# Kernel tuning notes

Hardware: AMD Instinct MI355X
Metric: run time of the kernel (lower is better)

Reference implementation:

```python
import jax, jax.numpy as jnp
import numpy as np

C = 512
NUM_HEADS = 8
HEAD_DIM = C // NUM_HEADS


def setup_inputs() -> dict:
    key = jax.random.key(0)
    ks = jax.random.split(key, 9)
    s = 1.0 / np.sqrt(C)
    x = jax.random.normal(ks[0], (8, C, 32, 32), dtype=jnp.float32)
    Wq = jax.random.uniform(ks[1], (C, C), jnp.float32, -s, s)
    bq = jax.random.uniform(ks[2], (C,), jnp.float32, -s, s)
    Wk = jax.random.uniform(ks[3], (C, C), jnp.float32, -s, s)
    bk = jax.random.uniform(ks[4], (C,), jnp.float32, -s, s)
    Wv = jax.random.uniform(ks[5], (C, C), jnp.float32, -s, s)
    bv = jax.random.uniform(ks[6], (C,), jnp.float32, -s, s)
    Wo = jax.random.uniform(ks[7], (C, C), jnp.float32, -s, s)
    bo = jax.random.uniform(ks[8], (C,), jnp.float32, -s, s)
    return {"x": x, "Wq": Wq, "bq": bq, "Wk": Wk, "bk": bk,
            "Wv": Wv, "bv": bv, "Wo": Wo, "bo": bo}


def reference(x, Wq, bq, Wk, bk, Wv, bv, Wo, bo):
    N, Cc, H, W = x.shape
    S = H * W
    # [N, S, C] token sequence
    xs = x.reshape(N, Cc, S).transpose(0, 2, 1)
    # torch Linear: y = x @ W^T + b
    q = xs @ Wq.T + bq
    k = xs @ Wk.T + bk
    v = xs @ Wv.T + bv
    # [N, h, S, d]
    q = q.reshape(N, S, NUM_HEADS, HEAD_DIM).transpose(0, 2, 1, 3)
    k = k.reshape(N, S, NUM_HEADS, HEAD_DIM).transpose(0, 2, 1, 3)
    v = v.reshape(N, S, NUM_HEADS, HEAD_DIM).transpose(0, 2, 1, 3)
    energy = jnp.einsum('nhqd,nhkd->nhqk', q, k)
    attn = jax.nn.softmax(energy / np.sqrt(HEAD_DIM), axis=3)
    out = jnp.einsum('nhql,nhld->nhqd', attn, v)
    # back to [N, S, C]; note torch reshape from (N,h,S,d) order
    out = out.reshape(N, Cc, S) if False else out.reshape(N, -1, Cc)
    out = out @ Wo.T + bo
    return out.reshape(N, Cc, H, W)


if __name__ == "__main__":
    o = reference(**setup_inputs())
    print(o.shape)
```

## Files before the change

kernel.cpp:

```cpp
#include <hip/hip_runtime.h>


typedef _Float16 f16x8 __attribute__((ext_vector_type(8)));
typedef _Float16 f16x4 __attribute__((ext_vector_type(4)));
typedef float f32x4 __attribute__((ext_vector_type(4)));

__device__ inline void gl_lds16(const void* g, void* l) {
  __builtin_amdgcn_global_load_lds((const __attribute__((address_space(1))) void*)g,
                                   (__attribute__((address_space(3))) void*)l, 16, 0, 0);
}

__device__ inline float fexp2(float x) {
#if __has_builtin(__builtin_amdgcn_exp2f)
  return __builtin_amdgcn_exp2f(x);
#else
  return exp2f(x);
#endif
}

__global__ void prep(const float* __restrict__ x,
                     const float* __restrict__ Wq, const float* __restrict__ bq,
                     const float* __restrict__ Wk, const float* __restrict__ bk,
                     const float* __restrict__ Wv, const float* __restrict__ bv,
                     const float* __restrict__ Wo,
                     _Float16* __restrict__ xs16, _Float16* __restrict__ Wqkv16,
                     float* __restrict__ bqkv, _Float16* __restrict__ Wo16) {
  __shared__ float t[32][33];
  const int tid = threadIdx.x;
  if (blockIdx.x < 1024) {
    const float g = 0.18033688011112042f;
    int i = blockIdx.x * 256 + tid;
    Wqkv16[i]          = (_Float16)(Wq[i] * g);
    Wqkv16[262144 + i] = (_Float16)Wk[i];
    Wqkv16[524288 + i] = (_Float16)Wv[i];
    Wo16[i]            = (_Float16)Wo[i];
    if (i < 512) {
      bqkv[i]        = bq[i] * g;
      bqkv[512 + i]  = bk[i];
      bqkv[1024 + i] = bv[i];
    }
    return;
  }
  const int bid = blockIdx.x - 1024;
  const int n = bid >> 9, c0 = ((bid >> 5) & 15) * 32, s0 = (bid & 31) * 32;
  const int tx = tid & 31, ty = tid >> 5;
#pragma unroll
  for (int i = 0; i < 4; ++i) {
    int cc = ty + i * 8;
    t[cc][tx] = x[((size_t)n * 512 + c0 + cc) * 1024 + s0 + tx];
  }
  __syncthreads();
#pragma unroll
  for (int i = 0; i < 4; ++i) {
    int ss = ty + i * 8;
    xs16[((size_t)n * 1024 + s0 + ss) * 512 + c0 + tx] = (_Float16)t[tx][ss];
  }
}

__global__ __launch_bounds__(256, 2) void qkv_gemm(
    const _Float16* __restrict__ A, const _Float16* __restrict__ Bw,
    const float* __restrict__ bias, _Float16* __restrict__ QK,
    _Float16* __restrict__ Vt) {
  __shared__ _Float16 smem[16896];
  _Float16* As = smem;
  _Float16* Bs = smem + 4096;
  const int tid = threadIdx.x;
  const int lane = tid & 63, w = tid >> 6;
  const int quad = lane >> 4, l15 = lane & 15;
  const int bm = blockIdx.x * 128, bn = blockIdx.y * 128;
  const int wr = (w >> 1) * 64, wc = (w & 1) * 64;
  f32x4 acc[4][4] = {};
  for (int k0 = 0; k0 < 512; k0 += 32) {
    __syncthreads();
#pragma unroll
    for (int c = 0; c < 2; ++c) {
      int idx = c * 256 + tid;
      int row = idx >> 2, sc = idx & 3;
      int kg = sc ^ ((row >> 1) & 3);
      gl_lds16(A + (size_t)(bm + row) * 512 + k0 + kg * 8, As + idx * 8);
      gl_lds16(Bw + (size_t)(bn + row) * 512 + k0 + kg * 8, Bs + idx * 8);
    }
    __syncthreads();
    f16x8 af[4], bf[4];
#pragma unroll
    for (int i = 0; i < 4; ++i) {
      int ra = wr + i * 16 + l15;
      af[i] = *(const f16x8*)(As + ra * 32 + (quad ^ ((ra >> 1) & 3)) * 8);
      int rb = wc + i * 16 + l15;
      bf[i] = *(const f16x8*)(Bs + rb * 32 + (quad ^ ((rb >> 1) & 3)) * 8);
    }
#pragma unroll
    for (int i = 0; i < 4; ++i)
#pragma unroll
      for (int j = 0; j < 4; ++j)
        acc[i][j] = __builtin_amdgcn_mfma_f32_16x16x32_f16(af[i], bf[j], acc[i][j], 0, 0, 0);
  }
  if (blockIdx.y < 8) {
#pragma unroll
    for (int j = 0; j < 4; ++j) {
      int col = bn + wc + j * 16 + l15;
      float bb = bias[col];
#pragma unroll
      for (int i = 0; i < 4; ++i) {
        int rowb = bm + wr + i * 16 + quad * 4;
#pragma unroll
        for (int r = 0; r < 4; ++r)
          QK[(size_t)(rowb + r) * 1024 + col] = (_Float16)(acc[i][j][r] + bb);
      }
    }
  } else {
    __syncthreads();
#pragma unroll
    for (int j = 0; j < 4; ++j) {
      int cl = wc + j * 16 + l15;
      float bb = bias[bn + cl];
#pragma unroll
      for (int i = 0; i < 4; ++i) {
        int row = wr + i * 16 + quad * 4;
        f16x4 pk;
#pragma unroll
        for (int r = 0; r < 4; ++r) pk[r] = (_Float16)(acc[i][j][r] + bb);
        *(f16x4*)(smem + cl * 132 + row) = pk;
      }
    }
    __syncthreads();
    const int n = bm >> 10, s0g = bm & 1023;
    const int vh = (bn - 1024) >> 6;
    const int cl = tid >> 1, par = tid & 1;
    const int hh = vh + (cl >> 6), d = cl & 63;
    const size_t vrow = (((size_t)((n * 8 + hh) * 64 + d)) << 10) + s0g;
#pragma unroll
    for (int g = 0; g < 8; ++g) {
      int pb = g * 16 + par * 8;
      int a32 = pb & ~31, q = (pb >> 3) & 3;
      f16x4 lo = *(const f16x4*)(smem + cl * 132 + a32 + 4 * q);
      f16x4 hi = *(const f16x4*)(smem + cl * 132 + a32 + 16 + 4 * q);
      f16x8 o = {lo[0], lo[1], lo[2], lo[3], hi[0], hi[1], hi[2], hi[3]};
      *(f16x8*)(Vt + vrow + pb) = o;
    }
  }
}

__global__ __launch_bounds__(256, 2) void attn(
    const _Float16* __restrict__ QK, const _Float16* __restrict__ Vt,
    _Float16* __restrict__ O16) {
  __shared__ _Float16 Qs[128 * 64];
  __shared__ _Float16 Ks[128 * 64];
  __shared__ _Float16 Vs[64 * 128];
  const int tid = threadIdx.x, lane = tid & 63, w = tid >> 6;
  const int quad = lane >> 4, l15 = lane & 15;
  const int n = blockIdx.y >> 3, h = blockIdx.y & 7;
  const int q0 = blockIdx.x * 128;
#pragma unroll
  for (int c = 0; c < 4; ++c) {
    int idx = c * 256 + tid;
    int row = idx >> 3, sc = idx & 7;
    int dg = sc ^ (row & 7);
    gl_lds16(QK + (size_t)(n * 1024 + q0 + row) * 1024 + h * 64 + dg * 8, Qs + idx * 8);
  }
  __syncthreads();
  f16x8 qf[2][2];
#pragma unroll
  for (int mt = 0; mt < 2; ++mt)
#pragma unroll
    for (int dc = 0; dc < 2; ++dc) {
      int row = w * 32 + mt * 16 + l15;
      qf[mt][dc] = *(const f16x8*)(Qs + row * 64 + ((dc * 4 + quad) ^ (row & 7)) * 8);
    }
  f32x4 oacc[2][4] = {};
  f32x4 lsum[2] = {};
  const f16x8 ones = {(_Float16)1, (_Float16)1, (_Float16)1, (_Float16)1,
                      (_Float16)1, (_Float16)1, (_Float16)1, (_Float16)1};

  for (int kt = 0; kt < 8; ++kt) {
    __syncthreads();
#pragma unroll
    for (int c = 0; c < 4; ++c) {
      int idx = c * 256 + tid;
      int row = idx >> 3, sck = idx & 7;
      int dg = sck ^ (row & 7);
      gl_lds16(QK + (size_t)(n * 1024 + kt * 128 + row) * 1024 + 512 + h * 64 + dg * 8,
               Ks + idx * 8);
      int d = idx >> 4, scv = idx & 15;
      int vg = scv ^ (d & 7);
      gl_lds16(Vt + (size_t)((n * 8 + h) * 64 + d) * 1024 + kt * 128 + vg * 8,
               Vs + idx * 8);
    }
    __syncthreads();
#pragma unroll
    for (int sc = 0; sc < 4; ++sc) {
      f32x4 sacc[2][2] = {};
#pragma unroll
      for (int t = 0; t < 2; ++t) {
        int rk = (sc * 2 + t) * 16 + l15;
        f16x8 kf0 = *(const f16x8*)(Ks + rk * 64 + ((quad) ^ (rk & 7)) * 8);
        f16x8 kf1 = *(const f16x8*)(Ks + rk * 64 + ((4 + quad) ^ (rk & 7)) * 8);
#pragma unroll
        for (int mt = 0; mt < 2; ++mt) {
          sacc[mt][t] = __builtin_amdgcn_mfma_f32_16x16x32_f16(kf0, qf[mt][0], sacc[mt][t], 0, 0, 0);
          sacc[mt][t] = __builtin_amdgcn_mfma_f32_16x16x32_f16(kf1, qf[mt][1], sacc[mt][t], 0, 0, 0);
        }
      }
      f16x8 pf[2];
#pragma unroll
      for (int mt = 0; mt < 2; ++mt) {
#pragma unroll
        for (int t = 0; t < 2; ++t)
#pragma unroll
          for (int r = 0; r < 4; ++r)
            pf[mt][t * 4 + r] = (_Float16)fexp2(sacc[mt][t][r]);
        lsum[mt] = __builtin_amdgcn_mfma_f32_16x16x32_f16(pf[mt], ones, lsum[mt], 0, 0, 0);
      }
#pragma unroll
      for (int nt = 0; nt < 4; ++nt) {
        int rd = nt * 16 + l15;
        f16x8 vf = *(const f16x8*)(Vs + rd * 128 + ((sc * 4 + quad) ^ (rd & 7)) * 8);
#pragma unroll
        for (int mt = 0; mt < 2; ++mt)
          oacc[mt][nt] = __builtin_amdgcn_mfma_f32_16x16x32_f16(pf[mt], vf, oacc[mt][nt], 0, 0, 0);
      }
    }
  }
#pragma unroll
  for (int mt = 0; mt < 2; ++mt) {
#pragma unroll
    for (int r = 0; r < 4; ++r) {
      float rinv = 1.0f / lsum[mt][r];
      int s = q0 + w * 32 + mt * 16 + quad * 4 + r;
      int i = h * 128 + (s >> 3);
      int jb = (s & 7) * 64;
#pragma unroll
      for (int nt = 0; nt < 4; ++nt) {
        int d = nt * 16 + l15;
        O16[(size_t)(n * 1024 + i) * 512 + jb + d] = (_Float16)(oacc[mt][nt][r] * rinv);
      }
    }
  }
}

__global__ __launch_bounds__(256, 2) void out_gemm(
    const _Float16* __restrict__ A, const _Float16* __restrict__ Bw,
    const float* __restrict__ bias, float* __restrict__ out) {
  __shared__ _Float16 As[128 * 32];
  __shared__ _Float16 Bs[128 * 32];
  const int tid = threadIdx.x;
  const int lane = tid & 63, w = tid >> 6;
  const int quad = lane >> 4, l15 = lane & 15;
  const int bm = blockIdx.x * 128, bn = blockIdx.y * 128;
  const int wr = (w >> 1) * 64, wc = (w & 1) * 64;
  f32x4 acc[4][4] = {};
  for (int k0 = 0; k0 < 512; k0 += 32) {
    __syncthreads();
#pragma unroll
    for (int c = 0; c < 2; ++c) {
      int idx = c * 256 + tid;
      int row = idx >> 2, sc = idx & 3;
      int kg = sc ^ ((row >> 1) & 3);
      gl_lds16(A + (size_t)(bm + row) * 512 + k0 + kg * 8, As + idx * 8);
      gl_lds16(Bw + (size_t)(bn + row) * 512 + k0 + kg * 8, Bs + idx * 8);
    }
    __syncthreads();
    f16x8 af[4], bf[4];
#pragma unroll
    for (int i = 0; i < 4; ++i) {
      int ra = wr + i * 16 + l15;
      af[i] = *(const f16x8*)(As + ra * 32 + (quad ^ ((ra >> 1) & 3)) * 8);
      int rb = wc + i * 16 + l15;
      bf[i] = *(const f16x8*)(Bs + rb * 32 + (quad ^ ((rb >> 1) & 3)) * 8);
    }
#pragma unroll
    for (int i = 0; i < 4; ++i)
#pragma unroll
      for (int j = 0; j < 4; ++j)
        acc[i][j] = __builtin_amdgcn_mfma_f32_16x16x32_f16(af[i], bf[j], acc[i][j], 0, 0, 0);
  }
#pragma unroll
  for (int j = 0; j < 4; ++j) {
    int col = bn + wc + j * 16 + l15;
    float bb = bias[col];
#pragma unroll
    for (int i = 0; i < 4; ++i) {
      int rowb = bm + wr + i * 16 + quad * 4;
#pragma unroll
      for (int r = 0; r < 4; ++r)
        out[(size_t)(rowb + r) * 512 + col] = acc[i][j][r] + bb;
    }
  }
}

extern "C" void kernel_launch(void* const* d_in, const int* in_sizes, int n_in,
                              void* d_out, int out_size, void* d_ws, size_t ws_size,
                              hipStream_t stream) {
  const float* x  = (const float*)d_in[0];
  const float* Wq = (const float*)d_in[1];
  const float* bq = (const float*)d_in[2];
  const float* Wk = (const float*)d_in[3];
  const float* bk = (const float*)d_in[4];
  const float* Wv = (const float*)d_in[5];
  const float* bv = (const float*)d_in[6];
  const float* Wo = (const float*)d_in[7];
  const float* bo = (const float*)d_in[8];
  float* out = (float*)d_out;
  char* ws = (char*)d_ws;

  _Float16* xs16   = (_Float16*)(ws);
  _Float16* QK     = (_Float16*)(ws + (8u << 20));
  _Float16* Vt     = (_Float16*)(ws + (24u << 20));
  _Float16* Wqkv16 = (_Float16*)(ws + (32u << 20));
  _Float16* Wo16   = (_Float16*)(ws + (32u << 20) + 1572864);
  float*    bqkv   = (float*)   (ws + (32u << 20) + 2097152);

  hipLaunchKernelGGL(prep, dim3(5120), dim3(256), 0, stream,
                     x, Wq, bq, Wk, bk, Wv, bv, Wo, xs16, Wqkv16, bqkv, Wo16);
  hipLaunchKernelGGL(qkv_gemm, dim3(64, 12), dim3(256), 0, stream,
                     xs16, Wqkv16, bqkv, QK, Vt);
  hipLaunchKernelGGL(attn, dim3(8, 64), dim3(256), 0, stream, QK, Vt, xs16);
  hipLaunchKernelGGL(out_gemm, dim3(64, 4), dim3(256), 0, stream,
                     xs16, Wo16, bo, out);
}
```

Baseline: 144.6 us.

## Fuse fp32-to-fp16 conversion and transpose into GEMMs, dropping prep kernel

Removes the separate prep kernel. The QKV GEMM now reads fp32 x and weights directly, transposes and converts them in registers, and writes them to double-buffered LDS, prefetching the next K slice. The output GEMM likewise converts Wo on the fly and double-buffers A. The attention epilogue swaps the MFMA operand order so each lane writes vectorized f16x4 outputs, using a shuffle to fetch row sums. This saves a launch and a round trip of the converted data through memory, at the cost of more register pressure and repeated weight conversion in every block.

Measured after the change: 163.5 us. 1.13x slower.

```diff
diff --git a/kernel.cpp b/kernel.cpp
--- a/kernel.cpp
+++ b/kernel.cpp
@@ -3,6 +3,7 @@
 
 typedef _Float16 f16x8 __attribute__((ext_vector_type(8)));
 typedef _Float16 f16x4 __attribute__((ext_vector_type(4)));
+typedef _Float16 f16x2 __attribute__((ext_vector_type(2)));
 typedef float f32x4 __attribute__((ext_vector_type(4)));
 
 __device__ inline void gl_lds16(const void* g, void* l) {
@@ -18,69 +19,80 @@
 #endif
 }
 
-__global__ void prep(const float* __restrict__ x,
-                     const float* __restrict__ Wq, const float* __restrict__ bq,
-                     const float* __restrict__ Wk, const float* __restrict__ bk,
-                     const float* __restrict__ Wv, const float* __restrict__ bv,
-                     const float* __restrict__ Wo,
-                     _Float16* __restrict__ xs16, _Float16* __restrict__ Wqkv16,
-                     float* __restrict__ bqkv, _Float16* __restrict__ Wo16) {
-  __shared__ float t[32][33];
-  const int tid = threadIdx.x;
-  if (blockIdx.x < 1024) {
-    const float g = 0.18033688011112042f;
-    int i = blockIdx.x * 256 + tid;
-    Wqkv16[i]          = (_Float16)(Wq[i] * g);
-    Wqkv16[262144 + i] = (_Float16)Wk[i];
-    Wqkv16[524288 + i] = (_Float16)Wv[i];
-    Wo16[i]            = (_Float16)Wo[i];
-    if (i < 512) {
-      bqkv[i]        = bq[i] * g;
-      bqkv[512 + i]  = bk[i];
-      bqkv[1024 + i] = bv[i];
-    }
-    return;
-  }
-  const int bid = blockIdx.x - 1024;
-  const int n = bid >> 9, c0 = ((bid >> 5) & 15) * 32, s0 = (bid & 31) * 32;
-  const int tx = tid & 31, ty = tid >> 5;
-#pragma unroll
-  for (int i = 0; i < 4; ++i) {
-    int cc = ty + i * 8;
-    t[cc][tx] = x[((size_t)n * 512 + c0 + cc) * 1024 + s0 + tx];
-  }
-  __syncthreads();
-#pragma unroll
-  for (int i = 0; i < 4; ++i) {
-    int ss = ty + i * 8;
-    xs16[((size_t)n * 1024 + s0 + ss) * 512 + c0 + tx] = (_Float16)t[tx][ss];
-  }
-}
-
 __global__ __launch_bounds__(256, 2) void qkv_gemm(
-    const _Float16* __restrict__ A, const _Float16* __restrict__ Bw,
-    const float* __restrict__ bias, _Float16* __restrict__ QK,
-    _Float16* __restrict__ Vt) {
+    const float* __restrict__ x,
+    const float* __restrict__ Wq, const float* __restrict__ Wk,
+    const float* __restrict__ Wv,
+    const float* __restrict__ bq, const float* __restrict__ bk,
+    const float* __restrict__ bv,
+    _Float16* __restrict__ QK, _Float16* __restrict__ Vt) {
   __shared__ _Float16 smem[16896];
-  _Float16* As = smem;
-  _Float16* Bs = smem + 4096;
   const int tid = threadIdx.x;
   const int lane = tid & 63, w = tid >> 6;
   const int quad = lane >> 4, l15 = lane & 15;
-  const int bm = blockIdx.x * 128, bn = blockIdx.y * 128;
+  const int bn = blockIdx.x * 128, bm = blockIdx.y * 128;
   const int wr = (w >> 1) * 64, wc = (w & 1) * 64;
+  const int n = bm >> 10, s_base = bm & 1023;
+  const float g = 0.18033688011112042f;
+  const float* Wsel = (bn < 512) ? Wq : (bn < 1024 ? Wk : Wv);
+  const float* bsel = (bn < 512) ? bq : (bn < 1024 ? bk : bv);
+  const int row0 = bn & 511;
+  const float gw = (bn < 512) ? g : 1.0f;
+
+  const int cpr = (tid >> 4) * 2;
+  const int s8 = (tid & 15) * 8;
+  const int wrow = tid >> 1;
+  const int wh = (tid & 1) * 16;
+
+  float av[16], wv16[16];
   f32x4 acc[4][4] = {};
-  for (int k0 = 0; k0 < 512; k0 += 32) {
-    __syncthreads();
+
+  {
+    const float* xs = x + ((size_t)(n * 512 + cpr) * 1024) + s_base + s8;
+    *(float4*)(av + 0) = *(const float4*)(xs);
+    *(float4*)(av + 4) = *(const float4*)(xs + 4);
+    *(float4*)(av + 8) = *(const float4*)(xs + 1024);
+    *(float4*)(av + 12) = *(const float4*)(xs + 1028);
+    const float* ws = Wsel + (size_t)(row0 + wrow) * 512 + wh;
+    *(float4*)(wv16 + 0) = *(const float4*)(ws);
+    *(float4*)(wv16 + 4) = *(const float4*)(ws + 4);
+    *(float4*)(wv16 + 8) = *(const float4*)(ws + 8);
+    *(float4*)(wv16 + 12) = *(const float4*)(ws + 12);
+  }
+  for (int ki = 0; ki < 16; ++ki) {
+    const int buf = ki & 1;
+    _Float16* As = smem + buf * 8192;
+    _Float16* Bs = smem + buf * 8192 + 4096;
+#pragma unroll
+    for (int i = 0; i < 8; ++i) {
+      int s_l = s8 + i;
+      int slot = (cpr >> 3) ^ ((s_l >> 1) & 3);
+      f16x2 pk = {(_Float16)av[i], (_Float16)av[8 + i]};
+      *(f16x2*)(As + s_l * 32 + slot * 8 + (cpr & 7)) = pk;
+    }
 #pragma unroll
     for (int c = 0; c < 2; ++c) {
-      int idx = c * 256 + tid;
-      int row = idx >> 2, sc = idx & 3;
-      int kg = sc ^ ((row >> 1) & 3);
-      gl_lds16(A + (size_t)(bm + row) * 512 + k0 + kg * 8, As + idx * 8);
-      gl_lds16(Bw + (size_t)(bn + row) * 512 + k0 + kg * 8, Bs + idx * 8);
-    }
-    __syncthreads();
+      int jc = (tid & 1) * 2 + c;
+      int slot = jc ^ ((wrow >> 1) & 3);
+      f16x8 pk;
+#pragma unroll
+      for (int j = 0; j < 8; ++j) pk[j] = (_Float16)(wv16[c * 8 + j] * gw);
+      *(f16x8*)(Bs + wrow * 32 + slot * 8) = pk;
+    }
+    __syncthreads();
+    if (ki < 15) {
+      int k0 = (ki + 1) * 32;
+      const float* xs = x + ((size_t)(n * 512 + k0 + cpr) * 1024) + s_base + s8;
+      *(float4*)(av + 0) = *(const float4*)(xs);
+      *(float4*)(av + 4) = *(const float4*)(xs + 4);
+      *(float4*)(av + 8) = *(const float4*)(xs + 1024);
+      *(float4*)(av + 12) = *(const float4*)(xs + 1028);
+      const float* ws = Wsel + (size_t)(row0 + wrow) * 512 + k0 + wh;
+      *(float4*)(wv16 + 0) = *(const float4*)(ws);
+      *(float4*)(wv16 + 4) = *(const float4*)(ws + 4);
+      *(float4*)(wv16 + 8) = *(const float4*)(ws + 8);
+      *(float4*)(wv16 + 12) = *(const float4*)(ws + 12);
+    }
     f16x8 af[4], bf[4];
 #pragma unroll
     for (int i = 0; i < 4; ++i) {
@@ -94,12 +106,14 @@
 #pragma unroll
       for (int j = 0; j < 4; ++j)
         acc[i][j] = __builtin_amdgcn_mfma_f32_16x16x32_f16(af[i], bf[j], acc[i][j], 0, 0, 0);
-  }
-  if (blockIdx.y < 8) {
+    __syncthreads();
+  }
+  if (bn < 1024) {
 #pragma unroll
     for (int j = 0; j < 4; ++j) {
-      int col = bn + wc + j * 16 + l15;
-      float bb = bias[col];
+      int cl = wc + j * 16 + l15;
+      float bb = bsel[(bn & 511) + cl] * gw;
+      int col = bn + cl;
 #pragma unroll
       for (int i = 0; i < 4; ++i) {
         int rowb = bm + wr + i * 16 + quad * 4;
@@ -113,7 +127,7 @@
 #pragma unroll
     for (int j = 0; j < 4; ++j) {
       int cl = wc + j * 16 + l15;
-      float bb = bias[bn + cl];
+      float bb = bsel[cl + (bn & 511)];
 #pragma unroll
       for (int i = 0; i < 4; ++i) {
         int row = wr + i * 16 + quad * 4;
@@ -124,14 +138,14 @@
       }
     }
     __syncthreads();
-    const int n = bm >> 10, s0g = bm & 1023;
+    const int s0g = bm & 1023;
     const int vh = (bn - 1024) >> 6;
     const int cl = tid >> 1, par = tid & 1;
     const int hh = vh + (cl >> 6), d = cl & 63;
     const size_t vrow = (((size_t)((n * 8 + hh) * 64 + d)) << 10) + s0g;
 #pragma unroll
-    for (int g = 0; g < 8; ++g) {
-      int pb = g * 16 + par * 8;
+    for (int gq = 0; gq < 8; ++gq) {
+      int pb = gq * 16 + par * 8;
       int a32 = pb & ~31, q = (pb >> 3) & 3;
       f16x4 lo = *(const f16x4*)(smem + cl * 132 + a32 + 4 * q);
       f16x4 hi = *(const f16x4*)(smem + cl * 132 + a32 + 16 + 4 * q);
@@ -167,7 +181,7 @@
       int row = w * 32 + mt * 16 + l15;
       qf[mt][dc] = *(const f16x8*)(Qs + row * 64 + ((dc * 4 + quad) ^ (row & 7)) * 8);
     }
-  f32x4 oacc[2][4] = {};
+  f32x4 oaccT[4][2] = {};
   f32x4 lsum[2] = {};
   const f16x8 ones = {(_Float16)1, (_Float16)1, (_Float16)1, (_Float16)1,
                       (_Float16)1, (_Float16)1, (_Float16)1, (_Float16)1};
@@ -217,49 +231,88 @@
         f16x8 vf = *(const f16x8*)(Vs + rd * 128 + ((sc * 4 + quad) ^ (rd & 7)) * 8);
 #pragma unroll
         for (int mt = 0; mt < 2; ++mt)
-          oacc[mt][nt] = __builtin_amdgcn_mfma_f32_16x16x32_f16(pf[mt], vf, oacc[mt][nt], 0, 0, 0);
+          oaccT[nt][mt] = __builtin_amdgcn_mfma_f32_16x16x32_f16(vf, pf[mt], oaccT[nt][mt], 0, 0, 0);
       }
     }
   }
 #pragma unroll
   for (int mt = 0; mt < 2; ++mt) {
-#pragma unroll
-    for (int r = 0; r < 4; ++r) {
-      float rinv = 1.0f / lsum[mt][r];
-      int s = q0 + w * 32 + mt * 16 + quad * 4 + r;
-      int i = h * 128 + (s >> 3);
-      int jb = (s & 7) * 64;
-#pragma unroll
-      for (int nt = 0; nt < 4; ++nt) {
-        int d = nt * 16 + l15;
-        O16[(size_t)(n * 1024 + i) * 512 + jb + d] = (_Float16)(oacc[mt][nt][r] * rinv);
-      }
+    int r3 = l15 & 3;
+    float lv = lsum[mt][0];
+    lv = (r3 == 1) ? lsum[mt][1] : lv;
+    lv = (r3 == 2) ? lsum[mt][2] : lv;
+    lv = (r3 == 3) ? lsum[mt][3] : lv;
+    float lq = __shfl(lv, (l15 >> 2) * 16 + (l15 & 3), 64);
+    float rinv = 1.0f / lq;
+    int q = q0 + w * 32 + mt * 16 + l15;
+    int i = h * 128 + (q >> 3);
+    size_t base = (size_t)(n * 1024 + i) * 512 + (q & 7) * 64 + quad * 4;
+#pragma unroll
+    for (int nt = 0; nt < 4; ++nt) {
+      f16x4 pk;
+#pragma unroll
+      for (int r = 0; r < 4; ++r) pk[r] = (_Float16)(oaccT[nt][mt][r] * rinv);
+      *(f16x4*)(O16 + base + nt * 16) = pk;
     }
   }
 }
 
 __global__ __launch_bounds__(256, 2) void out_gemm(
-    const _Float16* __restrict__ A, const _Float16* __restrict__ Bw,
-    const float* __restrict__ bias, float* __restrict__ out) {
-  __shared__ _Float16 As[128 * 32];
-  __shared__ _Float16 Bs[128 * 32];
+    const _Float16* __restrict__ A, const float* __restrict__ Wo,
+    const float* __restrict__ bo, float* __restrict__ out) {
+  __shared__ _Float16 smem[16384];
   const int tid = threadIdx.x;
   const int lane = tid & 63, w = tid >> 6;
   const int quad = lane >> 4, l15 = lane & 15;
   const int bm = blockIdx.x * 128, bn = blockIdx.y * 128;
   const int wr = (w >> 1) * 64, wc = (w & 1) * 64;
+  const int wrow = tid >> 1, wh = (tid & 1) * 16;
+  float wv16[16];
   f32x4 acc[4][4] = {};
-  for (int k0 = 0; k0 < 512; k0 += 32) {
-    __syncthreads();
+  {
 #pragma unroll
     for (int c = 0; c < 2; ++c) {
       int idx = c * 256 + tid;
       int row = idx >> 2, sc = idx & 3;
       int kg = sc ^ ((row >> 1) & 3);
-      gl_lds16(A + (size_t)(bm + row) * 512 + k0 + kg * 8, As + idx * 8);
-      gl_lds16(Bw + (size_t)(bn + row) * 512 + k0 + kg * 8, Bs + idx * 8);
-    }
-    __syncthreads();
+      gl_lds16(A + (size_t)(bm + row) * 512 + kg * 8, smem + idx * 8);
+    }
+    const float* ws = Wo + (size_t)(bn + wrow) * 512 + wh;
+    *(float4*)(wv16 + 0) = *(const float4*)(ws);
+    *(float4*)(wv16 + 4) = *(const float4*)(ws + 4);
+    *(float4*)(wv16 + 8) = *(const float4*)(ws + 8);
+    *(float4*)(wv16 + 12) = *(const float4*)(ws + 12);
+  }
+  for (int ki = 0; ki < 16; ++ki) {
+    const int buf = ki & 1;
+    _Float16* As = smem + buf * 8192;
+    _Float16* Bs = smem + buf * 8192 + 4096;
+#pragma unroll
+    for (int c = 0; c < 2; ++c) {
+      int jc = (tid & 1) * 2 + c;
+      int slot = jc ^ ((wrow >> 1) & 3);
+      f16x8 pk;
+#pragma unroll
+      for (int j = 0; j < 8; ++j) pk[j] = (_Float16)wv16[c * 8 + j];
+      *(f16x8*)(Bs + wrow * 32 + slot * 8) = pk;
+    }
+    __syncthreads();
+    if (ki < 15) {
+      int k0 = (ki + 1) * 32;
+      _Float16* Asn = smem + (1 - buf) * 8192;
+#pragma unroll
+      for (int c = 0; c < 2; ++c) {
+        int idx = c * 256 + tid;
+        int row = idx >> 2, sc = idx & 3;
+        int kg = sc ^ ((row >> 1) & 3);
+        gl_lds16(A + (size_t)(bm + row) * 512 + k0 + kg * 8, Asn + idx * 8);
+      }
+      const float* ws = Wo + (size_t)(bn + wrow) * 512 + k0 + wh;
+      *(float4*)(wv16 + 0) = *(const float4*)(ws);
+      *(float4*)(wv16 + 4) = *(const float4*)(ws + 4);
+      *(float4*)(wv16 + 8) = *(const float4*)(ws + 8);
+      *(float4*)(wv16 + 12) = *(const float4*)(ws + 12);
+    }
     f16x8 af[4], bf[4];
 #pragma unroll
     for (int i = 0; i < 4; ++i) {
@@ -273,11 +326,12 @@
 #pragma unroll
       for (int j = 0; j < 4; ++j)
         acc[i][j] = __builtin_amdgcn_mfma_f32_16x16x32_f16(af[i], bf[j], acc[i][j], 0, 0, 0);
+    __syncthreads();
   }
 #pragma unroll
   for (int j = 0; j < 4; ++j) {
     int col = bn + wc + j * 16 + l15;
-    float bb = bias[col];
+    float bb = bo[col];
 #pragma unroll
     for (int i = 0; i < 4; ++i) {
       int rowb = bm + wr + i * 16 + quad * 4;
@@ -303,18 +357,13 @@
   float* out = (float*)d_out;
   char* ws = (char*)d_ws;
 
-  _Float16* xs16   = (_Float16*)(ws);
-  _Float16* QK     = (_Float16*)(ws + (8u << 20));
-  _Float16* Vt     = (_Float16*)(ws + (24u << 20));
-  _Float16* Wqkv16 = (_Float16*)(ws + (32u << 20));
-  _Float16* Wo16   = (_Float16*)(ws + (32u << 20) + 1572864);
-  float*    bqkv   = (float*)   (ws + (32u << 20) + 2097152);
-
-  hipLaunchKernelGGL(prep, dim3(5120), dim3(256), 0, stream,
-                     x, Wq, bq, Wk, bk, Wv, bv, Wo, xs16, Wqkv16, bqkv, Wo16);
-  hipLaunchKernelGGL(qkv_gemm, dim3(64, 12), dim3(256), 0, stream,
-                     xs16, Wqkv16, bqkv, QK, Vt);
-  hipLaunchKernelGGL(attn, dim3(8, 64), dim3(256), 0, stream, QK, Vt, xs16);
+  _Float16* QK  = (_Float16*)(ws);
+  _Float16* Vt  = (_Float16*)(ws + (16u << 20));
+  _Float16* O16 = (_Float16*)(ws + (24u << 20));
+
+  hipLaunchKernelGGL(qkv_gemm, dim3(12, 64), dim3(256), 0, stream,
+                     x, Wq, Wk, Wv, bq, bk, bv, QK, Vt);
+  hipLaunchKernelGGL(attn, dim3(8, 64), dim3(256), 0, stream, QK, Vt, O16);
   hipLaunchKernelGGL(out_gemm, dim3(64, 4), dim3(256), 0, stream,
-                     xs16, Wo16, bo, out);
-}
+                     O16, Wo, bo, out);
+}
```

## Store Q/K/V in MFMA-fragment-packed layout and drop LDS staging in attention

Applied to the files above, without the earlier changes.

The QKV GEMM epilogue now writes Q, K and V into per-head buffers pre-swizzled in the exact order the MFMA fragments are consumed. The attention kernel can then load each fragment straight from global memory with one contiguous 16-byte load per lane, with no LDS staging and no barriers. The PV product is also transposed so the output can be written as packed f16x4 stores, with the row sums moved across lanes by a shuffle. In exchange K and V are reread from global or L2 by every wave without LDS sharing, and the epilogue does scattered LDS gathers. The attention output also gets its own buffer instead of overwriting xs16.

Result: slower. 168.0 us (+16.2%).

```diff
diff --git a/kernel.cpp b/kernel.cpp
--- a/kernel.cpp
+++ b/kernel.cpp
@@ -59,8 +59,8 @@
 
 __global__ __launch_bounds__(256, 2) void qkv_gemm(
     const _Float16* __restrict__ A, const _Float16* __restrict__ Bw,
-    const float* __restrict__ bias, _Float16* __restrict__ QK,
-    _Float16* __restrict__ Vt) {
+    const float* __restrict__ bias, _Float16* __restrict__ Qp,
+    _Float16* __restrict__ Kp, _Float16* __restrict__ Vp) {
   __shared__ _Float16 smem[16896];
   _Float16* As = smem;
   _Float16* Bs = smem + 4096;
@@ -95,106 +95,92 @@
       for (int j = 0; j < 4; ++j)
         acc[i][j] = __builtin_amdgcn_mfma_f32_16x16x32_f16(af[i], bf[j], acc[i][j], 0, 0, 0);
   }
-  if (blockIdx.y < 8) {
-#pragma unroll
-    for (int j = 0; j < 4; ++j) {
-      int col = bn + wc + j * 16 + l15;
-      float bb = bias[col];
-#pragma unroll
-      for (int i = 0; i < 4; ++i) {
-        int rowb = bm + wr + i * 16 + quad * 4;
-#pragma unroll
-        for (int r = 0; r < 4; ++r)
-          QK[(size_t)(rowb + r) * 1024 + col] = (_Float16)(acc[i][j][r] + bb);
+  __syncthreads();
+#pragma unroll
+  for (int j = 0; j < 4; ++j) {
+    int cl = wc + j * 16 + l15;
+    float bb = bias[bn + cl];
+#pragma unroll
+    for (int i = 0; i < 4; ++i) {
+      int row = wr + i * 16 + quad * 4;
+      f16x4 pk;
+#pragma unroll
+      for (int r = 0; r < 4; ++r) pk[r] = (_Float16)(acc[i][j][r] + bb);
+      *(f16x4*)(smem + cl * 132 + row) = pk;
+    }
+  }
+  __syncthreads();
+  const int cls = bn >> 9;
+  const int h0 = (bn & 511) >> 6;
+  const int n = bm >> 10, s_base = bm & 1023;
+  _Float16* dst = (cls == 0) ? Qp : (cls == 1) ? Kp : Vp;
+  if (cls < 2) {
+#pragma unroll
+    for (int c = 0; c < 8; ++c) {
+      int id = c * 256 + tid;
+      int l15p = id & 15, qd = (id >> 4) & 3, th = (id >> 6) & 1;
+      int s16l = (id >> 7) & 7, h2 = id >> 10;
+      int f_loc = h2 * 64 + th * 32 + qd * 8;
+      int s_loc = s16l * 16 + l15p;
+      f16x8 v;
+#pragma unroll
+      for (int j = 0; j < 8; ++j) v[j] = smem[(f_loc + j) * 132 + s_loc];
+      size_t off = (size_t)(n * 8 + h0 + h2) * 65536 +
+                   (size_t)((s_base >> 4) + s16l) * 1024 + th * 512 + qd * 128 + l15p * 8;
+      *(f16x8*)(dst + off) = v;
+    }
+  } else {
+    const int kt = s_base >> 7;
+#pragma unroll
+    for (int c = 0; c < 8; ++c) {
+      int id = c * 256 + tid;
+      int l15d = id & 15, qd = (id >> 4) & 3, nt = (id >> 6) & 3;
+      int sc = (id >> 8) & 3, h2 = id >> 10;
+      int f_loc = h2 * 64 + nt * 16 + l15d;
+      f16x8 v;
+#pragma unroll
+      for (int j = 0; j < 8; ++j) {
+        int s_loc = sc * 32 + (j >> 2) * 16 + qd * 4 + (j & 3);
+        v[j] = smem[f_loc * 132 + s_loc];
       }
-    }
-  } else {
-    __syncthreads();
-#pragma unroll
-    for (int j = 0; j < 4; ++j) {
-      int cl = wc + j * 16 + l15;
-      float bb = bias[bn + cl];
-#pragma unroll
-      for (int i = 0; i < 4; ++i) {
-        int row = wr + i * 16 + quad * 4;
-        f16x4 pk;
-#pragma unroll
-        for (int r = 0; r < 4; ++r) pk[r] = (_Float16)(acc[i][j][r] + bb);
-        *(f16x4*)(smem + cl * 132 + row) = pk;
-      }
-    }
-    __syncthreads();
-    const int n = bm >> 10, s0g = bm & 1023;
-    const int vh = (bn - 1024) >> 6;
-    const int cl = tid >> 1, par = tid & 1;
-    const int hh = vh + (cl >> 6), d = cl & 63;
-    const size_t vrow = (((size_t)((n * 8 + hh) * 64 + d)) << 10) + s0g;
-#pragma unroll
-    for (int g = 0; g < 8; ++g) {
-      int pb = g * 16 + par * 8;
-      int a32 = pb & ~31, q = (pb >> 3) & 3;
-      f16x4 lo = *(const f16x4*)(smem + cl * 132 + a32 + 4 * q);
-      f16x4 hi = *(const f16x4*)(smem + cl * 132 + a32 + 16 + 4 * q);
-      f16x8 o = {lo[0], lo[1], lo[2], lo[3], hi[0], hi[1], hi[2], hi[3]};
-      *(f16x8*)(Vt + vrow + pb) = o;
+      size_t off = (size_t)(n * 8 + h0 + h2) * 65536 + kt * 8192 +
+                   sc * 2048 + nt * 512 + qd * 128 + l15d * 8;
+      *(f16x8*)(dst + off) = v;
     }
   }
 }
 
 __global__ __launch_bounds__(256, 2) void attn(
-    const _Float16* __restrict__ QK, const _Float16* __restrict__ Vt,
-    _Float16* __restrict__ O16) {
-  __shared__ _Float16 Qs[128 * 64];
-  __shared__ _Float16 Ks[128 * 64];
-  __shared__ _Float16 Vs[64 * 128];
+    const _Float16* __restrict__ Qp, const _Float16* __restrict__ Kp,
+    const _Float16* __restrict__ Vp, _Float16* __restrict__ O16) {
   const int tid = threadIdx.x, lane = tid & 63, w = tid >> 6;
   const int quad = lane >> 4, l15 = lane & 15;
-  const int n = blockIdx.y >> 3, h = blockIdx.y & 7;
+  const int nh = blockIdx.y;
+  const int n = nh >> 3, h = nh & 7;
   const int q0 = blockIdx.x * 128;
-#pragma unroll
-  for (int c = 0; c < 4; ++c) {
-    int idx = c * 256 + tid;
-    int row = idx >> 3, sc = idx & 7;
-    int dg = sc ^ (row & 7);
-    gl_lds16(QK + (size_t)(n * 1024 + q0 + row) * 1024 + h * 64 + dg * 8, Qs + idx * 8);
-  }
-  __syncthreads();
+  const _Float16* Qb = Qp + (size_t)nh * 65536;
+  const _Float16* Kb = Kp + (size_t)nh * 65536;
+  const _Float16* Vb = Vp + (size_t)nh * 65536;
+  const int LL = lane * 8;
   f16x8 qf[2][2];
 #pragma unroll
   for (int mt = 0; mt < 2; ++mt)
 #pragma unroll
-    for (int dc = 0; dc < 2; ++dc) {
-      int row = w * 32 + mt * 16 + l15;
-      qf[mt][dc] = *(const f16x8*)(Qs + row * 64 + ((dc * 4 + quad) ^ (row & 7)) * 8);
-    }
-  f32x4 oacc[2][4] = {};
+    for (int th = 0; th < 2; ++th)
+      qf[mt][th] = *(const f16x8*)(Qb + (q0 / 16 + w * 2 + mt) * 1024 + th * 512 + LL);
+  f32x4 oaccT[4][2] = {};
   f32x4 lsum[2] = {};
   const f16x8 ones = {(_Float16)1, (_Float16)1, (_Float16)1, (_Float16)1,
                       (_Float16)1, (_Float16)1, (_Float16)1, (_Float16)1};
-
   for (int kt = 0; kt < 8; ++kt) {
-    __syncthreads();
-#pragma unroll
-    for (int c = 0; c < 4; ++c) {
-      int idx = c * 256 + tid;
-      int row = idx >> 3, sck = idx & 7;
-      int dg = sck ^ (row & 7);
-      gl_lds16(QK + (size_t)(n * 1024 + kt * 128 + row) * 1024 + 512 + h * 64 + dg * 8,
-               Ks + idx * 8);
-      int d = idx >> 4, scv = idx & 15;
-      int vg = scv ^ (d & 7);
-      gl_lds16(Vt + (size_t)((n * 8 + h) * 64 + d) * 1024 + kt * 128 + vg * 8,
-               Vs + idx * 8);
-    }
-    __syncthreads();
 #pragma unroll
     for (int sc = 0; sc < 4; ++sc) {
       f32x4 sacc[2][2] = {};
 #pragma unroll
       for (int t = 0; t < 2; ++t) {
-        int rk = (sc * 2 + t) * 16 + l15;
-        f16x8 kf0 = *(const f16x8*)(Ks + rk * 64 + ((quad) ^ (rk & 7)) * 8);
-        f16x8 kf1 = *(const f16x8*)(Ks + rk * 64 + ((4 + quad) ^ (rk & 7)) * 8);
+        int s16 = kt * 8 + sc * 2 + t;
+        f16x8 kf0 = *(const f16x8*)(Kb + s16 * 1024 + LL);
+        f16x8 kf1 = *(const f16x8*)(Kb + s16 * 1024 + 512 + LL);
 #pragma unroll
         for (int mt = 0; mt < 2; ++mt) {
           sacc[mt][t] = __builtin_amdgcn_mfma_f32_16x16x32_f16(kf0, qf[mt][0], sacc[mt][t], 0, 0, 0);
@@ -213,27 +199,31 @@
       }
 #pragma unroll
       for (int nt = 0; nt < 4; ++nt) {
-        int rd = nt * 16 + l15;
-        f16x8 vf = *(const f16x8*)(Vs + rd * 128 + ((sc * 4 + quad) ^ (rd & 7)) * 8);
+        f16x8 vf = *(const f16x8*)(Vb + kt * 8192 + sc * 2048 + nt * 512 + LL);
 #pragma unroll
         for (int mt = 0; mt < 2; ++mt)
-          oacc[mt][nt] = __builtin_amdgcn_mfma_f32_16x16x32_f16(pf[mt], vf, oacc[mt][nt], 0, 0, 0);
+          oaccT[nt][mt] = __builtin_amdgcn_mfma_f32_16x16x32_f16(vf, pf[mt], oaccT[nt][mt], 0, 0, 0);
       }
     }
   }
 #pragma unroll
   for (int mt = 0; mt < 2; ++mt) {
-#pragma unroll
-    for (int r = 0; r < 4; ++r) {
-      float rinv = 1.0f / lsum[mt][r];
-      int s = q0 + w * 32 + mt * 16 + quad * 4 + r;
-      int i = h * 128 + (s >> 3);
-      int jb = (s & 7) * 64;
-#pragma unroll
-      for (int nt = 0; nt < 4; ++nt) {
-        int d = nt * 16 + l15;
-        O16[(size_t)(n * 1024 + i) * 512 + jb + d] = (_Float16)(oacc[mt][nt][r] * rinv);
-      }
+    int r3 = l15 & 3;
+    float lv = lsum[mt][0];
+    lv = (r3 == 1) ? lsum[mt][1] : lv;
+    lv = (r3 == 2) ? lsum[mt][2] : lv;
+    lv = (r3 == 3) ? lsum[mt][3] : lv;
+    float lq = __shfl(lv, (l15 >> 2) * 16 + (l15 & 3), 64);
+    float rinv = 1.0f / lq;
+    int q = q0 + w * 32 + mt * 16 + l15;
+    int i = h * 128 + (q >> 3);
+    size_t base = (size_t)(n * 1024 + i) * 512 + (q & 7) * 64 + quad * 4;
+#pragma unroll
+    for (int nt = 0; nt < 4; ++nt) {
+      f16x4 pk;
+#pragma unroll
+      for (int r = 0; r < 4; ++r) pk[r] = (_Float16)(oaccT[nt][mt][r] * rinv);
+      *(f16x4*)(O16 + base + nt * 16) = pk;
     }
   }
 }
@@ -304,17 +294,19 @@
   char* ws = (char*)d_ws;
 
   _Float16* xs16   = (_Float16*)(ws);
-  _Float16* QK     = (_Float16*)(ws + (8u << 20));
-  _Float16* Vt     = (_Float16*)(ws + (24u << 20));
-  _Float16* Wqkv16 = (_Float16*)(ws + (32u << 20));
-  _Float16* Wo16   = (_Float16*)(ws + (32u << 20) + 1572864);
-  float*    bqkv   = (float*)   (ws + (32u << 20) + 2097152);
+  _Float16* O16    = (_Float16*)(ws + (8u << 20));
+  _Float16* Qp     = (_Float16*)(ws + (16u << 20));
+  _Float16* Kp     = (_Float16*)(ws + (24u << 20));
+  _Float16* Vp     = (_Float16*)(ws + (32u << 20));
+  _Float16* Wqkv16 = (_Float16*)(ws + (40u << 20));
+  _Float16* Wo16   = (_Float16*)(ws + (40u << 20) + 1572864);
+  float*    bqkv   = (float*)   (ws + (40u << 20) + 2097152);
 
   hipLaunchKernelGGL(prep, dim3(5120), dim3(256), 0, stream,
                      x, Wq, bq, Wk, bk, Wv, bv, Wo, xs16, Wqkv16, bqkv, Wo16);
   hipLaunchKernelGGL(qkv_gemm, dim3(64, 12), dim3(256), 0, stream,
-                     xs16, Wqkv16, bqkv, QK, Vt);
-  hipLaunchKernelGGL(attn, dim3(8, 64), dim3(256), 0, stream, QK, Vt, xs16);
+                     xs16, Wqkv16, bqkv, Qp, Kp, Vp);
+  hipLaunchKernelGGL(attn, dim3(8, 64), dim3(256), 0, stream, Qp, Kp, Vp, O16);
   hipLaunchKernelGGL(out_gemm, dim3(64, 4), dim3(256), 0, stream,
-                     xs16, Wo16, bo, out);
-}
+                     O16, Wo16, bo, out);
+}
```

## Deepen QKV GEMM k-tile to 64 and vectorize attention output stores

Applied to the files above, without the earlier changes.

The QKV projection GEMM now stages 64-wide K slices instead of 32, with a matching 8-way XOR swizzle. This halves the number of barrier and load rounds per tile and issues two MFMA sub-steps per stage. The attention kernel computes the transposed P·V product (V as the A operand), so each lane holds four consecutive head-dim values. It can then write packed f16x4 stores instead of scattered scalar halves, and the row sums are fetched with a lane shuffle. The larger LDS footprint per block could reduce occupancy.

After: 142.3 us. No clear change (-1.6%).

```diff
diff --git a/kernel.cpp b/kernel.cpp
--- a/kernel.cpp
+++ b/kernel.cpp
@@ -63,37 +63,40 @@
     _Float16* __restrict__ Vt) {
   __shared__ _Float16 smem[16896];
   _Float16* As = smem;
-  _Float16* Bs = smem + 4096;
+  _Float16* Bs = smem + 8192;
   const int tid = threadIdx.x;
   const int lane = tid & 63, w = tid >> 6;
   const int quad = lane >> 4, l15 = lane & 15;
   const int bm = blockIdx.x * 128, bn = blockIdx.y * 128;
   const int wr = (w >> 1) * 64, wc = (w & 1) * 64;
   f32x4 acc[4][4] = {};
-  for (int k0 = 0; k0 < 512; k0 += 32) {
-    __syncthreads();
-#pragma unroll
-    for (int c = 0; c < 2; ++c) {
+  for (int k0 = 0; k0 < 512; k0 += 64) {
+    __syncthreads();
+#pragma unroll
+    for (int c = 0; c < 4; ++c) {
       int idx = c * 256 + tid;
-      int row = idx >> 2, sc = idx & 3;
-      int kg = sc ^ ((row >> 1) & 3);
+      int row = idx >> 3, sc = idx & 7;
+      int kg = sc ^ (row & 7);
       gl_lds16(A + (size_t)(bm + row) * 512 + k0 + kg * 8, As + idx * 8);
       gl_lds16(Bw + (size_t)(bn + row) * 512 + k0 + kg * 8, Bs + idx * 8);
     }
     __syncthreads();
-    f16x8 af[4], bf[4];
-#pragma unroll
-    for (int i = 0; i < 4; ++i) {
-      int ra = wr + i * 16 + l15;
-      af[i] = *(const f16x8*)(As + ra * 32 + (quad ^ ((ra >> 1) & 3)) * 8);
-      int rb = wc + i * 16 + l15;
-      bf[i] = *(const f16x8*)(Bs + rb * 32 + (quad ^ ((rb >> 1) & 3)) * 8);
-    }
-#pragma unroll
-    for (int i = 0; i < 4; ++i)
-#pragma unroll
-      for (int j = 0; j < 4; ++j)
-        acc[i][j] = __builtin_amdgcn_mfma_f32_16x16x32_f16(af[i], bf[j], acc[i][j], 0, 0, 0);
+#pragma unroll
+    for (int kh = 0; kh < 2; ++kh) {
+      f16x8 af[4], bf[4];
+#pragma unroll
+      for (int i = 0; i < 4; ++i) {
+        int ra = wr + i * 16 + l15;
+        af[i] = *(const f16x8*)(As + ra * 64 + ((kh * 4 + quad) ^ (ra & 7)) * 8);
+        int rb = wc + i * 16 + l15;
+        bf[i] = *(const f16x8*)(Bs + rb * 64 + ((kh * 4 + quad) ^ (rb & 7)) * 8);
+      }
+#pragma unroll
+      for (int i = 0; i < 4; ++i)
+#pragma unroll
+        for (int j = 0; j < 4; ++j)
+          acc[i][j] = __builtin_amdgcn_mfma_f32_16x16x32_f16(af[i], bf[j], acc[i][j], 0, 0, 0);
+    }
   }
   if (blockIdx.y < 8) {
 #pragma unroll
@@ -167,7 +170,7 @@
       int row = w * 32 + mt * 16 + l15;
       qf[mt][dc] = *(const f16x8*)(Qs + row * 64 + ((dc * 4 + quad) ^ (row & 7)) * 8);
     }
-  f32x4 oacc[2][4] = {};
+  f32x4 oaccT[4][2] = {};
   f32x4 lsum[2] = {};
   const f16x8 ones = {(_Float16)1, (_Float16)1, (_Float16)1, (_Float16)1,
                       (_Float16)1, (_Float16)1, (_Float16)1, (_Float16)1};
@@ -217,23 +220,28 @@
         f16x8 vf = *(const f16x8*)(Vs + rd * 128 + ((sc * 4 + quad) ^ (rd & 7)) * 8);
 #pragma unroll
         for (int mt = 0; mt < 2; ++mt)
-          oacc[mt][nt] = __builtin_amdgcn_mfma_f32_16x16x32_f16(pf[mt], vf, oacc[mt][nt], 0, 0, 0);
+          oaccT[nt][mt] = __builtin_amdgcn_mfma_f32_16x16x32_f16(vf, pf[mt], oaccT[nt][mt], 0, 0, 0);
       }
     }
   }
 #pragma unroll
   for (int mt = 0; mt < 2; ++mt) {
-#pragma unroll
-    for (int r = 0; r < 4; ++r) {
-      float rinv = 1.0f / lsum[mt][r];
-      int s = q0 + w * 32 + mt * 16 + quad * 4 + r;
-      int i = h * 128 + (s >> 3);
-      int jb = (s & 7) * 64;
-#pragma unroll
-      for (int nt = 0; nt < 4; ++nt) {
-        int d = nt * 16 + l15;
-        O16[(size_t)(n * 1024 + i) * 512 + jb + d] = (_Float16)(oacc[mt][nt][r] * rinv);
-      }
+    int r3 = l15 & 3;
+    float lv = lsum[mt][0];
+    lv = (r3 == 1) ? lsum[mt][1] : lv;
+    lv = (r3 == 2) ? lsum[mt][2] : lv;
+    lv = (r3 == 3) ? lsum[mt][3] : lv;
+    float lq = __shfl(lv, (l15 >> 2) * 16 + (l15 & 3), 64);
+    float rinv = 1.0f / lq;
+    int q = q0 + w * 32 + mt * 16 + l15;
+    int i = h * 128 + (q >> 3);
+    size_t base = (size_t)(n * 1024 + i) * 512 + (q & 7) * 64 + quad * 4;
+#pragma unroll
+    for (int nt = 0; nt < 4; ++nt) {
+      f16x4 pk;
+#pragma unroll
+      for (int r = 0; r < 4; ++r) pk[r] = (_Float16)(oaccT[nt][mt][r] * rinv);
+      *(f16x4*)(O16 + base + nt * 16) = pk;
     }
   }
 }
```
